# Kernel tuning notes

Measured on AMD Instinct MI355X. Metric: run time of the kernel, lower is better.

The kernel has to match this reference:

```python
import jax, jax.numpy as jnp
import numpy as np


def setup_inputs() -> dict:
    key = jax.random.key(0)
    k1, k2 = jax.random.split(key)
    x = jax.random.normal(k1, (8, 128, 128, 128), dtype=jnp.float32)        # [N, C, H, W]
    codebook = jax.random.normal(k2, (256, 128), dtype=jnp.float32)         # [K, C] class_emb_vecs
    return {"x": x, "codebook": codebook}


def reference(x, codebook):
    # Brute-force 1-NN with p=2 (Euclidean), matching sklearn NearestNeighbors(brute, p=2).
    # argmin ||q - c||_2 == argmin (||q||^2 - 2 q.c + ||c||^2), so use the GEMM form.
    N, C, H, W = x.shape
    q = jnp.transpose(x, (0, 2, 3, 1)).reshape(-1, C)       # [N*H*W, C], matches x.reshape(-1, C) channel-last? 
    # NOTE: torch x.reshape(-1, C) on [N,C,H,W] flattens with C as the fastest-varying of the
    # leading dims only when memory layout is NCHW -> rows are (n, c_blocks)... Torch's
    # reshape(-1, C) actually slices contiguous groups of C elements along W. To be faithful
    # to x.reshape(-1, C) on a contiguous NCHW tensor:
    q = x.reshape(-1, C)                                     # [N*C*H*W/C, C] — same elements, same order as torch
    q_sq = jnp.sum(q * q, axis=1, keepdims=True)             # [M, 1]
    c_sq = jnp.sum(codebook * codebook, axis=1)              # [K]
    # squared distances: [M, K]
    d2 = q_sq - 2.0 * (q @ codebook.T) + c_sq[None, :]
    idx = jnp.argmin(d2, axis=1).astype(jnp.int32)           # [M]
    return idx.reshape(N, H, W)
```

## Files before the change

kernel.cpp:

```cpp
#include <hip/hip_runtime.h>
#include <hip/hip_bf16.h>


typedef __bf16 bf16x8 __attribute__((ext_vector_type(8)));
typedef float  floatx4 __attribute__((ext_vector_type(4)));

#define MFMA16 __builtin_amdgcn_mfma_f32_16x16x32_bf16

#define CNT_OFF 0
#define CSQ_OFF 1024
#define CBB_OFF 4096
#define WL_OFF  (4096 + 131072)
#define PBF_OFF (WL_OFF + WL_CAP * 4)
#define PBI_OFF (PBF_OFF + 2097152)
#define WL_CAP  32768
#define T_FLAG  0.004f

typedef __attribute__((address_space(1))) const unsigned int gu32;
typedef __attribute__((address_space(3))) unsigned int lu32;

__device__ __forceinline__ unsigned fmap(float f) {
    unsigned u = __float_as_uint(f);
    return (u & 0x80000000u) ? ~u : (u | 0x80000000u);
}

__global__ void knn_prep(const float* __restrict__ cb, __bf16* __restrict__ cbB,
                         float* __restrict__ csq, int* __restrict__ cnt) {
    const int tid = threadIdx.x;
    const int id = blockIdx.x * 256 + tid;
    if (id == 0) *cnt = 0;
    const int ln = id & 63;
    const int part = (id >> 6) & 1;
    const int step = id >> 7;
    const int t4 = step & 15;
    const int kb = step >> 4;
    const int n = t4 * 16 + (ln & 15);
    const int k0 = kb * 32 + (ln >> 4) * 8;
    const float* src = cb + (size_t)n * 128 + k0;
    union { __bf16 h[8]; uint4 u; } p;
#pragma unroll
    for (int j = 0; j < 8; ++j) {
        float f = src[j];
        __bf16 hh = (__bf16)f;
        p.h[j] = (part == 0) ? hh : (__bf16)(f - (float)hh);
    }
    *(uint4*)(cbB + (size_t)id * 8) = p.u;

    if (blockIdx.x == 0) {
        const float4* row = (const float4*)(cb + (size_t)tid * 128);
        float a0 = 0.f, a1 = 0.f, a2 = 0.f, a3 = 0.f;
#pragma unroll 8
        for (int j = 0; j < 32; ++j) {
            float4 v = row[j];
            a0 = fmaf(v.x, v.x, a0);
            a1 = fmaf(v.y, v.y, a1);
            a2 = fmaf(v.z, v.z, a2);
            a3 = fmaf(v.w, v.w, a3);
        }
        csq[tid] = (a0 + a1) + (a2 + a3);
    }
}

__global__ __launch_bounds__(1024, 4) void knn_mfma(const float* __restrict__ x,
                                                    const __bf16* __restrict__ cbB,
                                                    const float* __restrict__ csq_g,
                                                    float2* __restrict__ pbf,
                                                    int* __restrict__ pbi) {
    __shared__ __bf16 sB[65536];

    const int tid = threadIdx.x;
    const int wave = tid >> 6;
    const int lane = tid & 63;
    const int rl = lane & 15;
    const int kg = lane >> 4;
    const int pair = wave >> 1;
    const int half = wave & 1;

    {
        const char* gsrc = (const char*)cbB + wave * 8192 + lane * 16;
        char* ldst = (char*)sB + wave * 8192;
#pragma unroll
        for (int i = 0; i < 8; ++i)
            __builtin_amdgcn_global_load_lds((gu32*)(gsrc + i * 1024),
                                             (lu32*)(ldst + i * 1024), 16, 0, 0);
    }

    float cs[8];
#pragma unroll
    for (int tt = 0; tt < 8; ++tt) cs[tt] = csq_g[(half * 8 + tt) * 16 + rl];

#pragma unroll 1
    for (int bt = 0; bt < 4; ++bt) {
        const size_t q0 = (size_t)blockIdx.x * 512 + bt * 128 + pair * 16;

        const float* xq = x + (q0 + rl) * 128 + kg * 8;
        bf16x8 ah[4], al[4];
#pragma unroll
        for (int kb = 0; kb < 4; ++kb) {
            float4 f0 = *(const float4*)(xq + kb * 32);
            float4 f1 = *(const float4*)(xq + kb * 32 + 4);
            float f[8] = {f0.x, f0.y, f0.z, f0.w, f1.x, f1.y, f1.z, f1.w};
            union { __bf16 h[8]; bf16x8 v; } phv, plv;
#pragma unroll
            for (int j = 0; j < 8; ++j) {
                __bf16 hh = (__bf16)f[j];
                phv.h[j] = hh;
                plv.h[j] = (__bf16)(f[j] - (float)hh);
            }
            ah[kb] = phv.v;
            al[kb] = plv.v;
        }

        floatx4 acc[8];
#pragma unroll
        for (int tt = 0; tt < 8; ++tt) acc[tt] = (floatx4){0.f, 0.f, 0.f, 0.f};

        if (bt == 0) __syncthreads();

#pragma unroll
        for (int kb = 0; kb < 4; ++kb) {
            const __bf16* sbase = sB + kb * 16384 + half * 8192 + lane * 8;
#pragma unroll
            for (int tt = 0; tt < 8; ++tt) {
                bf16x8 bh = *(const bf16x8*)(sbase + tt * 1024);
                bf16x8 bl = *(const bf16x8*)(sbase + tt * 1024 + 512);
                acc[tt] = MFMA16(ah[kb], bh, acc[tt], 0, 0, 0);
                acc[tt] = MFMA16(al[kb], bh, acc[tt], 0, 0, 0);
                acc[tt] = MFMA16(ah[kb], bl, acc[tt], 0, 0, 0);
            }
        }

#pragma unroll
        for (int r = 0; r < 4; ++r) {
            float bf = __builtin_inff(), sf = __builtin_inff();
            int bi = 0;
#pragma unroll
            for (int tt = 0; tt < 8; ++tt) {
                const float sc = fmaf(-2.0f, acc[tt][r], cs[tt]);
                const bool lt = sc < bf;
                sf = lt ? bf : fminf(sf, sc);
                bf = lt ? sc : bf;
                bi = lt ? ((half * 8 + tt) * 16 + rl) : bi;
            }
#pragma unroll
            for (int d = 1; d < 16; d <<= 1) {
                const float obf = __shfl_xor(bf, d);
                const int   obi = __shfl_xor(bi, d);
                const float osf = __shfl_xor(sf, d);
                const bool lt = obf < bf;
                const float loser = lt ? bf : obf;
                sf = fminf(fminf(sf, osf), loser);
                bf = lt ? obf : bf;
                bi = lt ? obi : bi;
            }
            if (rl == 0) {
                const size_t qg = q0 + kg * 4 + r;
                pbf[qg * 2 + half] = (float2){bf, sf};
                pbi[qg * 2 + half] = bi;
            }
        }
    }
}

__global__ __launch_bounds__(256) void knn_merge(const float2* __restrict__ pbf,
                                                 const int* __restrict__ pbi,
                                                 int* __restrict__ out,
                                                 int* __restrict__ cnt,
                                                 int* __restrict__ wl) {
    const int q = blockIdx.x * 256 + threadIdx.x;
    const float4 v = *(const float4*)(pbf + (size_t)q * 2);
    const int2  iv = *(const int2*)(pbi + (size_t)q * 2);
    const bool w0 = v.x < v.z;
    const float B = w0 ? v.x : v.z;
    const float S = fminf(w0 ? v.y : v.w, w0 ? v.z : v.x);
    out[q] = w0 ? iv.x : iv.y;
    if (S - B < T_FLAG) {
        int idx = atomicAdd(cnt, 1);
        if (idx < WL_CAP) wl[idx] = q;
    }
}

__global__ __launch_bounds__(256) void knn_refine(const float* __restrict__ x,
                                                  const float* __restrict__ cb,
                                                  const float* __restrict__ csq_g,
                                                  const int* __restrict__ wl,
                                                  const int* __restrict__ cnt,
                                                  int* __restrict__ out) {
    __shared__ unsigned long long sP[4];
    const int tid = threadIdx.x;
    const int lane = tid & 63;
    const int wave = tid >> 6;

    int n = *cnt;
    if (n > WL_CAP) n = WL_CAP;
    const float mycsq = csq_g[tid];
    const float4* cr = (const float4*)(cb + (size_t)tid * 128);

    for (int i = blockIdx.x; i < n; i += gridDim.x) {
        const int q = wl[i];
        const float4* qr = (const float4*)(x + (size_t)q * 128);
        float a0 = 0.f, a1 = 0.f, a2 = 0.f, a3 = 0.f;
#pragma unroll 8
        for (int c4 = 0; c4 < 32; ++c4) {
            float4 qv = qr[c4];
            float4 cv = cr[c4];
            a0 = fmaf(qv.x, cv.x, a0);
            a1 = fmaf(qv.y, cv.y, a1);
            a2 = fmaf(qv.z, cv.z, a2);
            a3 = fmaf(qv.w, cv.w, a3);
        }
        float dot = (a0 + a1) + (a2 + a3);
        float score = fmaf(-2.0f, dot, mycsq);
        unsigned long long key =
            ((unsigned long long)fmap(score) << 32) | (unsigned)tid;
#pragma unroll
        for (int d = 1; d < 64; d <<= 1) {
            unsigned long long o = __shfl_xor(key, d);
            key = o < key ? o : key;
        }
        if (lane == 0) sP[wave] = key;
        __syncthreads();
        if (tid == 0) {
            unsigned long long b = sP[0];
            unsigned long long o;
            o = sP[1]; b = o < b ? o : b;
            o = sP[2]; b = o < b ? o : b;
            o = sP[3]; b = o < b ? o : b;
            out[q] = (int)(unsigned)(b & 0xFFFFFFFFull);
        }
        __syncthreads();
    }
}

extern "C" void kernel_launch(void* const* d_in, const int* in_sizes, int n_in,
                              void* d_out, int out_size, void* d_ws, size_t ws_size,
                              hipStream_t stream) {
    const float* x = (const float*)d_in[0];
    const float* cb = (const float*)d_in[1];
    int* out = (int*)d_out;

    char* ws = (char*)d_ws;
    int* cnt = (int*)(ws + CNT_OFF);
    float* csq = (float*)(ws + CSQ_OFF);
    __bf16* cbB = (__bf16*)(ws + CBB_OFF);
    int* wl = (int*)(ws + WL_OFF);
    float2* pbf = (float2*)(ws + PBF_OFF);
    int* pbi = (int*)(ws + PBI_OFF);

    const int M = in_sizes[0] / 128;

    knn_prep<<<32, 256, 0, stream>>>(cb, cbB, csq, cnt);
    knn_mfma<<<M / 512, 1024, 0, stream>>>(x, cbB, csq, pbf, pbi);
    knn_merge<<<M / 256, 256, 0, stream>>>(pbf, pbi, out, cnt, wl);
    knn_refine<<<240, 256, 0, stream>>>(x, cb, csq, wl, cnt, out);
}
```

Before: 126.8 us.

## Switch distance GEMM from 16x16x32 to 32x32x16 MFMA tiles

Replaces the 16x16x32 bf16 MFMA with the 32x32x16 variant, so each wave computes a 32-query by 128-code tile. The codebook fragment layout in the prep kernel, the LDS addressing, the per-lane row mapping and the shuffle reduction are all reworked to match, and the block shrinks from 1024 to 512 threads. The larger tile is meant to cut LDS reads of B per MFMA and raise the compute-to-load ratio. In exchange, each wave holds more accumulator and A-operand registers, has fewer waves per block, and runs a longer 32-lane argmin reduction.

```diff
diff --git a/kernel.cpp b/kernel.cpp
--- a/kernel.cpp
+++ b/kernel.cpp
@@ -3,17 +3,17 @@
 
 
 typedef __bf16 bf16x8 __attribute__((ext_vector_type(8)));
-typedef float  floatx4 __attribute__((ext_vector_type(4)));
-
-#define MFMA16 __builtin_amdgcn_mfma_f32_16x16x32_bf16
+typedef float  floatx16 __attribute__((ext_vector_type(16)));
+
+#define MFMA32 __builtin_amdgcn_mfma_f32_32x32x16_bf16
 
 #define CNT_OFF 0
 #define CSQ_OFF 1024
 #define CBB_OFF 4096
+#define WL_CAP  32768
 #define WL_OFF  (4096 + 131072)
 #define PBF_OFF (WL_OFF + WL_CAP * 4)
 #define PBI_OFF (PBF_OFF + 2097152)
-#define WL_CAP  32768
 #define T_FLAG  0.004f
 
 typedef __attribute__((address_space(1))) const unsigned int gu32;
@@ -31,11 +31,11 @@
     if (id == 0) *cnt = 0;
     const int ln = id & 63;
     const int part = (id >> 6) & 1;
-    const int step = id >> 7;
-    const int t4 = step & 15;
-    const int kb = step >> 4;
-    const int n = t4 * 16 + (ln & 15);
-    const int k0 = kb * 32 + (ln >> 4) * 8;
+    const int frag = id >> 7;
+    const int t32 = frag & 7;
+    const int ks = frag >> 3;
+    const int n = t32 * 32 + (ln & 31);
+    const int k0 = ks * 16 + (ln >> 5) * 8;
     const float* src = cb + (size_t)n * 128 + k0;
     union { __bf16 h[8]; uint4 u; } p;
 #pragma unroll
@@ -61,44 +61,44 @@
     }
 }
 
-__global__ __launch_bounds__(1024, 4) void knn_mfma(const float* __restrict__ x,
-                                                    const __bf16* __restrict__ cbB,
-                                                    const float* __restrict__ csq_g,
-                                                    float2* __restrict__ pbf,
-                                                    int* __restrict__ pbi) {
+__global__ __launch_bounds__(512, 2) void knn_mfma(const float* __restrict__ x,
+                                                   const __bf16* __restrict__ cbB,
+                                                   const float* __restrict__ csq_g,
+                                                   float2* __restrict__ pbf,
+                                                   int* __restrict__ pbi) {
     __shared__ __bf16 sB[65536];
 
     const int tid = threadIdx.x;
     const int wave = tid >> 6;
     const int lane = tid & 63;
-    const int rl = lane & 15;
-    const int kg = lane >> 4;
+    const int col = lane & 31;
+    const int hi = lane >> 5;
     const int pair = wave >> 1;
     const int half = wave & 1;
 
     {
-        const char* gsrc = (const char*)cbB + wave * 8192 + lane * 16;
-        char* ldst = (char*)sB + wave * 8192;
-#pragma unroll
-        for (int i = 0; i < 8; ++i)
+        const char* gsrc = (const char*)cbB + wave * 16384 + lane * 16;
+        char* ldst = (char*)sB + wave * 16384;
+#pragma unroll
+        for (int i = 0; i < 16; ++i)
             __builtin_amdgcn_global_load_lds((gu32*)(gsrc + i * 1024),
                                              (lu32*)(ldst + i * 1024), 16, 0, 0);
     }
 
-    float cs[8];
-#pragma unroll
-    for (int tt = 0; tt < 8; ++tt) cs[tt] = csq_g[(half * 8 + tt) * 16 + rl];
+    float cs[4];
+#pragma unroll
+    for (int tt = 0; tt < 4; ++tt) cs[tt] = csq_g[(half * 4 + tt) * 32 + col];
 
 #pragma unroll 1
     for (int bt = 0; bt < 4; ++bt) {
-        const size_t q0 = (size_t)blockIdx.x * 512 + bt * 128 + pair * 16;
-
-        const float* xq = x + (q0 + rl) * 128 + kg * 8;
-        bf16x8 ah[4], al[4];
-#pragma unroll
-        for (int kb = 0; kb < 4; ++kb) {
-            float4 f0 = *(const float4*)(xq + kb * 32);
-            float4 f1 = *(const float4*)(xq + kb * 32 + 4);
+        const size_t q0 = (size_t)blockIdx.x * 512 + bt * 128 + pair * 32;
+
+        const float* xq = x + (q0 + col) * 128 + hi * 8;
+        bf16x8 ah[8], al[8];
+#pragma unroll
+        for (int ks = 0; ks < 8; ++ks) {
+            float4 f0 = *(const float4*)(xq + ks * 16);
+            float4 f1 = *(const float4*)(xq + ks * 16 + 4);
             float f[8] = {f0.x, f0.y, f0.z, f0.w, f1.x, f1.y, f1.z, f1.w};
             union { __bf16 h[8]; bf16x8 v; } phv, plv;
 #pragma unroll
@@ -107,43 +107,45 @@
                 phv.h[j] = hh;
                 plv.h[j] = (__bf16)(f[j] - (float)hh);
             }
-            ah[kb] = phv.v;
-            al[kb] = plv.v;
-        }
-
-        floatx4 acc[8];
-#pragma unroll
-        for (int tt = 0; tt < 8; ++tt) acc[tt] = (floatx4){0.f, 0.f, 0.f, 0.f};
+            ah[ks] = phv.v;
+            al[ks] = plv.v;
+        }
+
+        floatx16 acc[4];
+#pragma unroll
+        for (int tt = 0; tt < 4; ++tt)
+#pragma unroll
+            for (int e = 0; e < 16; ++e) acc[tt][e] = 0.f;
 
         if (bt == 0) __syncthreads();
 
 #pragma unroll
-        for (int kb = 0; kb < 4; ++kb) {
-            const __bf16* sbase = sB + kb * 16384 + half * 8192 + lane * 8;
-#pragma unroll
-            for (int tt = 0; tt < 8; ++tt) {
+        for (int ks = 0; ks < 8; ++ks) {
+            const __bf16* sbase = sB + (ks * 8 + half * 4) * 1024 + lane * 8;
+#pragma unroll
+            for (int tt = 0; tt < 4; ++tt) {
                 bf16x8 bh = *(const bf16x8*)(sbase + tt * 1024);
                 bf16x8 bl = *(const bf16x8*)(sbase + tt * 1024 + 512);
-                acc[tt] = MFMA16(ah[kb], bh, acc[tt], 0, 0, 0);
-                acc[tt] = MFMA16(al[kb], bh, acc[tt], 0, 0, 0);
-                acc[tt] = MFMA16(ah[kb], bl, acc[tt], 0, 0, 0);
-            }
-        }
-
-#pragma unroll
-        for (int r = 0; r < 4; ++r) {
+                acc[tt] = MFMA32(ah[ks], bh, acc[tt], 0, 0, 0);
+                acc[tt] = MFMA32(al[ks], bh, acc[tt], 0, 0, 0);
+                acc[tt] = MFMA32(ah[ks], bl, acc[tt], 0, 0, 0);
+            }
+        }
+
+#pragma unroll
+        for (int r = 0; r < 16; ++r) {
             float bf = __builtin_inff(), sf = __builtin_inff();
             int bi = 0;
 #pragma unroll
-            for (int tt = 0; tt < 8; ++tt) {
+            for (int tt = 0; tt < 4; ++tt) {
                 const float sc = fmaf(-2.0f, acc[tt][r], cs[tt]);
                 const bool lt = sc < bf;
                 sf = lt ? bf : fminf(sf, sc);
                 bf = lt ? sc : bf;
-                bi = lt ? ((half * 8 + tt) * 16 + rl) : bi;
-            }
-#pragma unroll
-            for (int d = 1; d < 16; d <<= 1) {
+                bi = lt ? ((half * 4 + tt) * 32 + col) : bi;
+            }
+#pragma unroll
+            for (int d = 1; d < 32; d <<= 1) {
                 const float obf = __shfl_xor(bf, d);
                 const int   obi = __shfl_xor(bi, d);
                 const float osf = __shfl_xor(sf, d);
@@ -153,8 +155,9 @@
                 bf = lt ? obf : bf;
                 bi = lt ? obi : bi;
             }
-            if (rl == 0) {
-                const size_t qg = q0 + kg * 4 + r;
+            if (col == 0) {
+                const int qrow = (r & 3) + 8 * (r >> 2) + 4 * hi;
+                const size_t qg = q0 + qrow;
                 pbf[qg * 2 + half] = (float2){bf, sf};
                 pbi[qg * 2 + half] = bi;
             }
@@ -250,7 +253,7 @@
     const int M = in_sizes[0] / 128;
 
     knn_prep<<<32, 256, 0, stream>>>(cb, cbB, csq, cnt);
-    knn_mfma<<<M / 512, 1024, 0, stream>>>(x, cbB, csq, pbf, pbi);
+    knn_mfma<<<M / 512, 512, 0, stream>>>(x, cbB, csq, pbf, pbi);
     knn_merge<<<M / 256, 256, 0, stream>>>(pbf, pbi, out, cnt, wl);
     knn_refine<<<240, 256, 0, stream>>>(x, cb, csq, wl, cnt, out);
 }
```

Result: slower. 141.1 us (+11.3%).

## Compute two 16-row query tiles per wave to reuse codebook LDS reads

Applied to the files above, without the earlier changes.

Halves the block to 512 threads and has each wave process 32 queries (two 16-row M tiles) instead of 16. Every B fragment loaded from LDS now feeds two sets of MFMAs, which halves LDS read traffic per MFMA. Each wave now stages twice as much of the codebook into LDS. The cost is doubled accumulator and A-fragment register use, and fewer waves per block, which may lower occupancy and latency hiding.

```diff
diff --git a/kernel.cpp b/kernel.cpp
--- a/kernel.cpp
+++ b/kernel.cpp
@@ -10,10 +10,10 @@
 #define CNT_OFF 0
 #define CSQ_OFF 1024
 #define CBB_OFF 4096
+#define WL_CAP  32768
 #define WL_OFF  (4096 + 131072)
 #define PBF_OFF (WL_OFF + WL_CAP * 4)
 #define PBI_OFF (PBF_OFF + 2097152)
-#define WL_CAP  32768
 #define T_FLAG  0.004f
 
 typedef __attribute__((address_space(1))) const unsigned int gu32;
@@ -61,12 +61,12 @@
     }
 }
 
-__global__ __launch_bounds__(1024, 4) void knn_mfma(const float* __restrict__ x,
-                                                    const __bf16* __restrict__ cbB,
-                                                    const float* __restrict__ csq_g,
-                                                    float2* __restrict__ pbf,
-                                                    int* __restrict__ pbi) {
-    __shared__ __bf16 sB[65536];
+__global__ __launch_bounds__(512, 2) void knn_mfma(const float* __restrict__ x,
+                                                   const __bf16* __restrict__ cbB,
+                                                   const float* __restrict__ csq_g,
+                                                   float2* __restrict__ pbf,
+                                                   int* __restrict__ pbi) {
+    __shared__ __bf16 sB[32768 * 2];
 
     const int tid = threadIdx.x;
     const int wave = tid >> 6;
@@ -77,10 +77,10 @@
     const int half = wave & 1;
 
     {
-        const char* gsrc = (const char*)cbB + wave * 8192 + lane * 16;
-        char* ldst = (char*)sB + wave * 8192;
-#pragma unroll
-        for (int i = 0; i < 8; ++i)
+        const char* gsrc = (const char*)cbB + wave * 16384 + lane * 16;
+        char* ldst = (char*)sB + wave * 16384;
+#pragma unroll
+        for (int i = 0; i < 16; ++i)
             __builtin_amdgcn_global_load_lds((gu32*)(gsrc + i * 1024),
                                              (lu32*)(ldst + i * 1024), 16, 0, 0);
     }
@@ -91,29 +91,35 @@
 
 #pragma unroll 1
     for (int bt = 0; bt < 4; ++bt) {
-        const size_t q0 = (size_t)blockIdx.x * 512 + bt * 128 + pair * 16;
-
-        const float* xq = x + (q0 + rl) * 128 + kg * 8;
-        bf16x8 ah[4], al[4];
-#pragma unroll
-        for (int kb = 0; kb < 4; ++kb) {
-            float4 f0 = *(const float4*)(xq + kb * 32);
-            float4 f1 = *(const float4*)(xq + kb * 32 + 4);
-            float f[8] = {f0.x, f0.y, f0.z, f0.w, f1.x, f1.y, f1.z, f1.w};
-            union { __bf16 h[8]; bf16x8 v; } phv, plv;
-#pragma unroll
-            for (int j = 0; j < 8; ++j) {
-                __bf16 hh = (__bf16)f[j];
-                phv.h[j] = hh;
-                plv.h[j] = (__bf16)(f[j] - (float)hh);
+        const size_t q0 = (size_t)blockIdx.x * 512 + bt * 128 + pair * 32;
+
+        const float* xq = x + q0 * 128;
+        bf16x8 ah[2][4], al[2][4];
+#pragma unroll
+        for (int m = 0; m < 2; ++m) {
+#pragma unroll
+            for (int kb = 0; kb < 4; ++kb) {
+                const float* s = xq + (size_t)(m * 16 + rl) * 128 + kb * 32 + kg * 8;
+                float4 f0 = *(const float4*)(s);
+                float4 f1 = *(const float4*)(s + 4);
+                float f[8] = {f0.x, f0.y, f0.z, f0.w, f1.x, f1.y, f1.z, f1.w};
+                union { __bf16 h[8]; bf16x8 v; } phv, plv;
+#pragma unroll
+                for (int j = 0; j < 8; ++j) {
+                    __bf16 hh = (__bf16)f[j];
+                    phv.h[j] = hh;
+                    plv.h[j] = (__bf16)(f[j] - (float)hh);
+                }
+                ah[m][kb] = phv.v;
+                al[m][kb] = plv.v;
             }
-            ah[kb] = phv.v;
-            al[kb] = plv.v;
-        }
-
-        floatx4 acc[8];
-#pragma unroll
-        for (int tt = 0; tt < 8; ++tt) acc[tt] = (floatx4){0.f, 0.f, 0.f, 0.f};
+        }
+
+        floatx4 acc[2][8];
+#pragma unroll
+        for (int m = 0; m < 2; ++m)
+#pragma unroll
+            for (int tt = 0; tt < 8; ++tt) acc[m][tt] = (floatx4){0.f, 0.f, 0.f, 0.f};
 
         if (bt == 0) __syncthreads();
 
@@ -124,39 +130,45 @@
             for (int tt = 0; tt < 8; ++tt) {
                 bf16x8 bh = *(const bf16x8*)(sbase + tt * 1024);
                 bf16x8 bl = *(const bf16x8*)(sbase + tt * 1024 + 512);
-                acc[tt] = MFMA16(ah[kb], bh, acc[tt], 0, 0, 0);
-                acc[tt] = MFMA16(al[kb], bh, acc[tt], 0, 0, 0);
-                acc[tt] = MFMA16(ah[kb], bl, acc[tt], 0, 0, 0);
+                acc[0][tt] = MFMA16(ah[0][kb], bh, acc[0][tt], 0, 0, 0);
+                acc[1][tt] = MFMA16(ah[1][kb], bh, acc[1][tt], 0, 0, 0);
+                acc[0][tt] = MFMA16(al[0][kb], bh, acc[0][tt], 0, 0, 0);
+                acc[1][tt] = MFMA16(al[1][kb], bh, acc[1][tt], 0, 0, 0);
+                acc[0][tt] = MFMA16(ah[0][kb], bl, acc[0][tt], 0, 0, 0);
+                acc[1][tt] = MFMA16(ah[1][kb], bl, acc[1][tt], 0, 0, 0);
             }
         }
 
 #pragma unroll
-        for (int r = 0; r < 4; ++r) {
-            float bf = __builtin_inff(), sf = __builtin_inff();
-            int bi = 0;
-#pragma unroll
-            for (int tt = 0; tt < 8; ++tt) {
-                const float sc = fmaf(-2.0f, acc[tt][r], cs[tt]);
-                const bool lt = sc < bf;
-                sf = lt ? bf : fminf(sf, sc);
-                bf = lt ? sc : bf;
-                bi = lt ? ((half * 8 + tt) * 16 + rl) : bi;
-            }
-#pragma unroll
-            for (int d = 1; d < 16; d <<= 1) {
-                const float obf = __shfl_xor(bf, d);
-                const int   obi = __shfl_xor(bi, d);
-                const float osf = __shfl_xor(sf, d);
-                const bool lt = obf < bf;
-                const float loser = lt ? bf : obf;
-                sf = fminf(fminf(sf, osf), loser);
-                bf = lt ? obf : bf;
-                bi = lt ? obi : bi;
-            }
-            if (rl == 0) {
-                const size_t qg = q0 + kg * 4 + r;
-                pbf[qg * 2 + half] = (float2){bf, sf};
-                pbi[qg * 2 + half] = bi;
+        for (int m = 0; m < 2; ++m) {
+#pragma unroll
+            for (int r = 0; r < 4; ++r) {
+                float bf = __builtin_inff(), sf = __builtin_inff();
+                int bi = 0;
+#pragma unroll
+                for (int tt = 0; tt < 8; ++tt) {
+                    const float sc = fmaf(-2.0f, acc[m][tt][r], cs[tt]);
+                    const bool lt = sc < bf;
+                    sf = lt ? bf : fminf(sf, sc);
+                    bf = lt ? sc : bf;
+                    bi = lt ? ((half * 8 + tt) * 16 + rl) : bi;
+                }
+#pragma unroll
+                for (int d = 1; d < 16; d <<= 1) {
+                    const float obf = __shfl_xor(bf, d);
+                    const int   obi = __shfl_xor(bi, d);
+                    const float osf = __shfl_xor(sf, d);
+                    const bool lt = obf < bf;
+                    const float loser = lt ? bf : obf;
+                    sf = fminf(fminf(sf, osf), loser);
+                    bf = lt ? obf : bf;
+                    bi = lt ? obi : bi;
+                }
+                if (rl == 0) {
+                    const size_t qg = q0 + m * 16 + kg * 4 + r;
+                    pbf[qg * 2 + half] = (float2){bf, sf};
+                    pbi[qg * 2 + half] = bi;
+                }
             }
         }
     }
@@ -250,7 +262,7 @@
     const int M = in_sizes[0] / 128;
 
     knn_prep<<<32, 256, 0, stream>>>(cb, cbB, csq, cnt);
-    knn_mfma<<<M / 512, 1024, 0, stream>>>(x, cbB, csq, pbf, pbi);
+    knn_mfma<<<M / 512, 512, 0, stream>>>(x, cbB, csq, pbf, pbi);
     knn_merge<<<M / 256, 256, 0, stream>>>(pbf, pbi, out, cnt, wl);
     knn_refine<<<240, 256, 0, stream>>>(x, cb, csq, wl, cnt, out);
 }
```

Result: slower. 132.7 us (+4.6%).
